# Optimization experiments

Measured on AMD Instinct MI355X. Metric: run time of the kernel, lower is better.

## Reference

```python
import jax, jax.numpy as jnp
import numpy as np

D_MODEL = 1024
D_HEAD = 64

def setup_inputs() -> dict:
    key = jax.random.key(0)
    ks = jax.random.split(key, 7)
    s = 1.0 / np.sqrt(D_MODEL)
    x = jax.random.normal(ks[0], (4, 4096, D_MODEL), dtype=jnp.float32)
    Wq = jax.random.uniform(ks[1], (D_MODEL, D_HEAD), jnp.float32, -s, s)
    bq = jax.random.uniform(ks[2], (D_HEAD,), jnp.float32, -s, s)
    Wk = jax.random.uniform(ks[3], (D_MODEL, D_HEAD), jnp.float32, -s, s)
    bk = jax.random.uniform(ks[4], (D_HEAD,), jnp.float32, -s, s)
    Wv = jax.random.uniform(ks[5], (D_MODEL, D_HEAD), jnp.float32, -s, s)
    bv = jax.random.uniform(ks[6], (D_HEAD,), jnp.float32, -s, s)
    return {"x": x, "Wq": Wq, "bq": bq, "Wk": Wk, "bk": bk, "Wv": Wv, "bv": bv}

def reference(x, Wq, bq, Wk, bk, Wv, bv):
    # x: [b, s, d_model] -> Q,K,V: [b, s, d_head]
    Q = jnp.einsum('bsd,dh->bsh', x, Wq) + bq
    K = jnp.einsum('bsd,dh->bsh', x, Wk) + bk
    V = jnp.einsum('bsd,dh->bsh', x, Wv) + bv
    scale = 1.0 / jnp.sqrt(jnp.asarray(D_HEAD, x.dtype))
    scores = jnp.einsum('bqh,bkh->bqk', Q, K) * scale  # [b, s, s]
    attn = jax.nn.softmax(scores, axis=-1)
    return jnp.einsum('bqk,bkh->bqh', attn, V)  # [b, s, d_head]
```

## Files before the change

### kernel.cpp

```cpp
#include <hip/hip_runtime.h>

typedef __bf16 bf16x8 __attribute__((ext_vector_type(8)));
typedef __bf16 bf16x4 __attribute__((ext_vector_type(4)));
typedef float f32x4 __attribute__((ext_vector_type(4)));
typedef unsigned short u16x8 __attribute__((ext_vector_type(8)));

union FragU { u16x8 u; bf16x8 b; };
union PackU { bf16x4 v; unsigned long long q; };

__device__ __forceinline__ unsigned short bfbits(float f) {
  __bf16 h = (__bf16)f;
  union { __bf16 h; unsigned short s; } cv; cv.h = h;
  return cv.s;
}

#define MFMA16(a, b, c) __builtin_amdgcn_mfma_f32_16x16x32_bf16((a), (b), (c), 0, 0, 0)

#define QSCALE 0.18033688011112042f

__global__ __launch_bounds__(256) void wt_kernel(
    const float* __restrict__ Wq, const float* __restrict__ Wk, const float* __restrict__ Wv,
    unsigned short* __restrict__ WF)
{
  const int m = blockIdx.x >> 5;
  const int c = blockIdx.x & 31;
  const float* W = (m == 0) ? Wq : ((m == 1) ? Wk : Wv);
  const int t = threadIdx.x >> 6;
  const int lane = threadIdx.x & 63;
  const int l15 = lane & 15;
  const int g = lane >> 4;
  unsigned short* dst = WF + ((((size_t)m * 32 + c) * 4 + t) * 64 + lane) * 8;
#pragma unroll
  for (int e = 0; e < 8; ++e)
    dst[e] = bfbits(W[(size_t)(32 * c + 8 * g + e) * 64 + (16 * t + l15)]);
}

__global__ __launch_bounds__(256, 1) void proj_kernel(
    const float* __restrict__ x, const unsigned short* __restrict__ WF,
    const float* __restrict__ bq, const float* __restrict__ bk, const float* __restrict__ bv,
    unsigned short* __restrict__ Qb, unsigned short* __restrict__ KF,
    unsigned short* __restrict__ VF)
{
  __shared__ __align__(16) unsigned short ldsW[4][6144];
  const int tid = threadIdx.x;
  const int lane = tid & 63;
  const int wid = tid >> 6;
  const int l15 = lane & 15;
  const int g = lane >> 4;
  const int row0 = blockIdx.x * 64 + wid * 16;

  f32x4 accQ[4], accK[4], accV[4];
  const f32x4 zero = {0.f, 0.f, 0.f, 0.f};
#pragma unroll
  for (int i = 0; i < 4; ++i) { accQ[i] = zero; accK[i] = zero; accV[i] = zero; }

  const float* xrow = x + (size_t)(row0 + l15) * 1024;
  f32x4 xx0[4], xx1[4];

#define WDMA(CC) { const int sl_ = (CC) & 3; \
    _Pragma("unroll") for (int m_ = 0; m_ < 3; ++m_) { \
      const unsigned short* gs_ = WF + ((((size_t)m_ * 32 + (CC)) * 4 + wid) * 64 + lane) * 8; \
      __builtin_amdgcn_global_load_lds( \
          (const __attribute__((address_space(1))) void*)gs_, \
          (__attribute__((address_space(3))) void*)&ldsW[sl_][(m_ * 4 + wid) * 512], \
          16, 0, 0); } }

#define PLDX(XB, C) { xx0[XB] = *(const f32x4*)(xrow + 32 * (C) + 8 * g); \
                      xx1[XB] = *(const f32x4*)(xrow + 32 * (C) + 8 * g + 4); }

#define SUBIT(CC, KK, WIMM, DOW, DOX) { \
    asm volatile("s_waitcnt vmcnt(" #WIMM ")" ::: "memory"); \
    __builtin_amdgcn_s_barrier(); \
    __builtin_amdgcn_sched_barrier(0); \
    if (DOW) WDMA((CC) + 3); \
    FragU xf; \
    _Pragma("unroll") for (int i_ = 0; i_ < 4; ++i_) { \
      xf.b[i_] = (__bf16)xx0[KK][i_]; xf.b[4 + i_] = (__bf16)xx1[KK][i_]; } \
    if (DOX) PLDX(KK, (CC) + 4); \
    { const int rs_ = (CC) & 3; \
      _Pragma("unroll") for (int t = 0; t < 4; ++t) { \
        const bf16x8 wq_ = *(const bf16x8*)&ldsW[rs_][(0 * 4 + t) * 512 + lane * 8]; \
        const bf16x8 wk_ = *(const bf16x8*)&ldsW[rs_][(1 * 4 + t) * 512 + lane * 8]; \
        const bf16x8 wv_ = *(const bf16x8*)&ldsW[rs_][(2 * 4 + t) * 512 + lane * 8]; \
        accQ[t] = MFMA16(xf.b, wq_, accQ[t]); \
        accK[t] = MFMA16(xf.b, wk_, accK[t]); \
        accV[t] = MFMA16(wv_, xf.b, accV[t]); } } }

  WDMA(0)
  __builtin_amdgcn_sched_barrier(0);
  WDMA(1) WDMA(2)
  PLDX(0, 0) PLDX(1, 1) PLDX(2, 2) PLDX(3, 3)

#pragma unroll 1
  for (int cb = 0; cb < 28; cb += 4) {
    SUBIT(cb + 0, 0, 10, 1, 1)
    SUBIT(cb + 1, 1, 10, 1, 1)
    SUBIT(cb + 2, 2, 10, 1, 1)
    SUBIT(cb + 3, 3, 10, 1, 1)
  }
  SUBIT(28, 0, 10, 1, 0)
  SUBIT(29, 1, 8, 0, 0)
  SUBIT(30, 2, 3, 0, 0)
  SUBIT(31, 3, 0, 0, 0)

  const int b = blockIdx.x >> 6;
  const int kt = blockIdx.x & 63;
  const int q0 = row0 & 4095;
  unsigned short* Qbase = Qb + (size_t)b * 4096 * 64;
#pragma unroll
  for (int t = 0; t < 4; ++t) {
    const int hh = 16 * t + l15;
    const float bqv = bq[hh];
#pragma unroll
    for (int r = 0; r < 4; ++r)
      Qbase[(size_t)(q0 + 4 * g + r) * 64 + hh] = bfbits((accQ[t][r] + bqv) * QSCALE);
  }
  unsigned short* KFb = KF + ((size_t)b * 64 + kt) * 4096;
  unsigned short* VFb = VF + ((size_t)b * 64 + kt) * 4096;
#pragma unroll
  for (int t = 0; t < 4; ++t) {
    const int hh = 16 * t + l15;
    const float bkv = bk[hh];
#pragma unroll
    for (int r = 0; r < 4; ++r) {
      KFb[(size_t)((wid * 2 + (t >> 1)) * 64 + (t & 1) * 32 + (l15 >> 3) * 16 + 4 * g + r) * 8 +
          (l15 & 7)] = bfbits(accK[t][r] + bkv);
      const int hv = 16 * t + 4 * g + r;
      VFb[(size_t)((t * 2 + (wid >> 1)) * 64 + (wid & 1) * 32 + (l15 >> 3) * 16 + 4 * g + r) * 8 +
          (l15 & 7)] = bfbits(accV[t][r] + bv[hv]);
    }
  }
}

__global__ __launch_bounds__(512, 2) void flash_kernel(
    const unsigned short* __restrict__ Qb, const unsigned short* __restrict__ KF,
    const unsigned short* __restrict__ VF, float* __restrict__ out)
{
  __shared__ __align__(16) unsigned char lds[36864];
  const int tid = threadIdx.x;
  const int lane = tid & 63;
  const int w = tid >> 6;
  const int qg = w >> 2;
  const int ks = w & 3;
  const int l15 = lane & 15;
  const int g = lane >> 4;
  const int bid = blockIdx.x;
  const int xcd = bid & 7;
  const int b = xcd >> 1;
  const int qt = (bid >> 3) * 2 + (xcd & 1);
  const int q0 = qt * 64 + qg * 32;

  const unsigned short* Qp = Qb + (size_t)b * 4096 * 64;
  const unsigned short* KFb = KF + (size_t)b * 262144;
  const unsigned short* VFb = VF + (size_t)b * 262144;

  const bf16x8 qfA0 = *(const bf16x8*)(Qp + (size_t)(q0 + l15) * 64 + 8 * g);
  const bf16x8 qfA1 = *(const bf16x8*)(Qp + (size_t)(q0 + l15) * 64 + 32 + 8 * g);
  const bf16x8 qfB0 = *(const bf16x8*)(Qp + (size_t)(q0 + 16 + l15) * 64 + 8 * g);
  const bf16x8 qfB1 = *(const bf16x8*)(Qp + (size_t)(q0 + 16 + l15) * 64 + 32 + 8 * g);

  f32x4 O_A[4], O_B[4];
  const f32x4 zero = {0.f, 0.f, 0.f, 0.f};
#pragma unroll
  for (int i = 0; i < 4; ++i) { O_A[i] = zero; O_B[i] = zero; }
  float mA = -INFINITY, lA = 0.f, mB = -INFINITY, lB = 0.f;
  unsigned short* PwA = (unsigned short*)lds + (w * 2 + 0) * 1152;
  unsigned short* PwB = (unsigned short*)lds + (w * 2 + 1) * 1152;

#define SM_HALF(S, mvar, lvar, OA, PW) { \
  float mt = fmaxf(fmaxf(S[0][0], S[0][1]), fmaxf(S[0][2], S[0][3])); \
  _Pragma("unroll") for (int t = 1; t < 4; ++t) \
    _Pragma("unroll") for (int r = 0; r < 4; ++r) mt = fmaxf(mt, S[t][r]); \
  mt = fmaxf(mt, __shfl_xor(mt, 16)); \
  mt = fmaxf(mt, __shfl_xor(mt, 32)); \
  if (!__all(mt <= mvar + 8.0f)) { \
    const float mnew = fmaxf(mvar, mt); \
    const float alpha = __builtin_amdgcn_exp2f(mvar - mnew); \
    mvar = mnew; lvar *= alpha; \
    _Pragma("unroll") for (int r = 0; r < 4; ++r) { \
      const float ar = __shfl(alpha, 4 * g + r); \
      OA[0][r] *= ar; OA[1][r] *= ar; OA[2][r] *= ar; OA[3][r] *= ar; } \
  } \
  float ps = 0.f; \
  _Pragma("unroll") for (int t = 0; t < 4; ++t) { \
    const float p0 = __builtin_amdgcn_exp2f(S[t][0] - mvar); \
    const float p1 = __builtin_amdgcn_exp2f(S[t][1] - mvar); \
    const float p2 = __builtin_amdgcn_exp2f(S[t][2] - mvar); \
    const float p3 = __builtin_amdgcn_exp2f(S[t][3] - mvar); \
    ps += (p0 + p1) + (p2 + p3); \
    PackU pk_; pk_.v[0] = (__bf16)p0; pk_.v[1] = (__bf16)p1; \
    pk_.v[2] = (__bf16)p2; pk_.v[3] = (__bf16)p3; \
    *(unsigned long long*)((PW) + l15 * 72 + 16 * t + 4 * g) = pk_.q; } \
  ps += __shfl_xor(ps, 16); \
  ps += __shfl_xor(ps, 32); \
  lvar += ps; }

#define FBODY(KT, KFC, KFN, DOLD) { \
    const unsigned short* Vt_ = VFb + (KT) * 4096; \
    bf16x8 vf[8]; \
    _Pragma("unroll") for (int j = 0; j < 8; ++j) \
      vf[j] = *(const bf16x8*)(Vt_ + (j * 64 + lane) * 8); \
    if (DOLD) { \
      const unsigned short* Ktn_ = KFb + ((KT) + 4) * 4096; \
      _Pragma("unroll") for (int j = 0; j < 8; ++j) \
        KFN[j] = *(const bf16x8*)(Ktn_ + (j * 64 + lane) * 8); \
    } \
    f32x4 S_A[4], S_B[4]; \
    _Pragma("unroll") for (int t = 0; t < 4; ++t) { \
      S_A[t] = zero; \
      S_A[t] = MFMA16(KFC[2 * t], qfA0, S_A[t]); \
      S_A[t] = MFMA16(KFC[2 * t + 1], qfA1, S_A[t]); \
      S_B[t] = zero; \
      S_B[t] = MFMA16(KFC[2 * t], qfB0, S_B[t]); \
      S_B[t] = MFMA16(KFC[2 * t + 1], qfB1, S_B[t]); \
    } \
    SM_HALF(S_A, mA, lA, O_A, PwA) \
    SM_HALF(S_B, mB, lB, O_B, PwB) \
    _Pragma("unroll") for (int s = 0; s < 2; ++s) { \
      const bf16x8 paA = *(const bf16x8*)(PwA + l15 * 72 + 32 * s + 8 * g); \
      const bf16x8 paB = *(const bf16x8*)(PwB + l15 * 72 + 32 * s + 8 * g); \
      _Pragma("unroll") for (int nt = 0; nt < 4; ++nt) { \
        O_A[nt] = MFMA16(paA, vf[2 * nt + s], O_A[nt]); \
        O_B[nt] = MFMA16(paB, vf[2 * nt + s], O_B[nt]); \
      } } }

  bf16x8 kfA[8], kfB[8];
  {
    const unsigned short* Kt0 = KFb + ks * 4096;
#pragma unroll
    for (int j = 0; j < 8; ++j) kfA[j] = *(const bf16x8*)(Kt0 + (j * 64 + lane) * 8);
  }
#pragma unroll 1
  for (int kt = ks; kt < 64; kt += 8) {
    FBODY(kt, kfA, kfB, 1)
    FBODY(kt + 4, kfB, kfA, (kt + 8 < 64))
  }

  float* O_l = (float*)lds;
  float* mlp = (float*)(lds + 34816);
  const int q = tid >> 4;
  const int h0 = (tid & 15) * 4;
  const int qh = q >> 4, qr = q & 15;

#pragma unroll 1
  for (int pass = 0; pass < 2; ++pass) {
    __syncthreads();
    if (qg == pass) {
#pragma unroll
      for (int nt = 0; nt < 4; ++nt)
#pragma unroll
        for (int r = 0; r < 4; ++r) {
          O_l[((ks * 2 + 0) * 16 + 4 * g + r) * 68 + 16 * nt + l15] = O_A[nt][r];
          O_l[((ks * 2 + 1) * 16 + 4 * g + r) * 68 + 16 * nt + l15] = O_B[nt][r];
        }
      if (g == 0) {
        mlp[((ks * 2 + 0) * 16 + l15) * 2] = mA; mlp[((ks * 2 + 0) * 16 + l15) * 2 + 1] = lA;
        mlp[((ks * 2 + 1) * 16 + l15) * 2] = mB; mlp[((ks * 2 + 1) * 16 + l15) * 2 + 1] = lB;
      }
    }
    __syncthreads();
    float M = -INFINITY;
#pragma unroll
    for (int s = 0; s < 4; ++s) M = fmaxf(M, mlp[((s * 2 + qh) * 16 + qr) * 2]);
    float L = 0.f;
    f32x4 a0 = zero;
#pragma unroll
    for (int s = 0; s < 4; ++s) {
      const int rowi = (s * 2 + qh) * 16 + qr;
      const float wgt = __builtin_amdgcn_exp2f(mlp[rowi * 2] - M);
      L += wgt * mlp[rowi * 2 + 1];
      const f32x4 o0 = *(const f32x4*)&O_l[rowi * 68 + h0];
#pragma unroll
      for (int i = 0; i < 4; ++i) a0[i] += wgt * o0[i];
    }
    const float inv = 1.0f / L;
    float* ob = out + ((size_t)b * 4096 + qt * 64 + pass * 32 + q) * 64 + h0;
    f32x4 r0 = {a0[0] * inv, a0[1] * inv, a0[2] * inv, a0[3] * inv};
    *(f32x4*)ob = r0;
  }
}

extern "C" void kernel_launch(void* const* d_in, const int* in_sizes, int n_in,
                              void* d_out, int out_size, void* d_ws, size_t ws_size,
                              hipStream_t stream) {
  const float* x  = (const float*)d_in[0];
  const float* Wq = (const float*)d_in[1];
  const float* bq = (const float*)d_in[2];
  const float* Wk = (const float*)d_in[3];
  const float* bk = (const float*)d_in[4];
  const float* Wv = (const float*)d_in[5];
  const float* bv = (const float*)d_in[6];

  char* ws = (char*)d_ws;
  unsigned short* WF = (unsigned short*)ws;
  unsigned short* Qb = (unsigned short*)(ws + (512u << 10));
  unsigned short* KF = (unsigned short*)(ws + (512u << 10) + (2u << 20));
  unsigned short* VF = (unsigned short*)(ws + (512u << 10) + (4u << 20));
  float* out = (float*)d_out;

  hipLaunchKernelGGL(wt_kernel,    dim3(96),  dim3(256), 0, stream, Wq, Wk, Wv, WF);
  hipLaunchKernelGGL(proj_kernel,  dim3(256), dim3(256), 0, stream, x, WF, bq, bk, bv, Qb, KF, VF);
  hipLaunchKernelGGL(flash_kernel, dim3(256), dim3(512), 0, stream, Qb, KF, VF, out);
}
```

Measured before the change: 55.34 us.

## Give each wave private triple-buffered weight LDS copies to drop block barriers

Each wave now DMA-loads all twelve weight fragments for a chunk into its own LDS region, triple-buffered, instead of the four waves sharing one cooperatively loaded copy. This removes the per-chunk s_barrier, so waves synchronise only on their own vmcnt. In exchange each wave issues four times as many global-to-LDS loads, LDS use triples, and prefetch depth drops from three chunks ahead to two. The loop is also fully unrolled.

```diff
diff --git a/kernel.cpp b/kernel.cpp
--- a/kernel.cpp
+++ b/kernel.cpp
@@ -41,7 +41,7 @@
     unsigned short* __restrict__ Qb, unsigned short* __restrict__ KF,
     unsigned short* __restrict__ VF)
 {
-  __shared__ __align__(16) unsigned short ldsW[4][6144];
+  __shared__ __align__(16) unsigned short ldsW[4][3][6144];
   const int tid = threadIdx.x;
   const int lane = tid & 63;
   const int wid = tid >> 6;
@@ -57,51 +57,50 @@
   const float* xrow = x + (size_t)(row0 + l15) * 1024;
   f32x4 xx0[4], xx1[4];
 
-#define WDMA(CC) { const int sl_ = (CC) & 3; \
-    _Pragma("unroll") for (int m_ = 0; m_ < 3; ++m_) { \
-      const unsigned short* gs_ = WF + ((((size_t)m_ * 32 + (CC)) * 4 + wid) * 64 + lane) * 8; \
+#define WDMA(CC) { \
+    _Pragma("unroll") for (int f_ = 0; f_ < 12; ++f_) { \
+      const int m_ = f_ >> 2, t_ = f_ & 3; \
+      const unsigned short* gs_ = WF + ((((size_t)m_ * 32 + (CC)) * 4 + t_) * 64 + lane) * 8; \
       __builtin_amdgcn_global_load_lds( \
           (const __attribute__((address_space(1))) void*)gs_, \
-          (__attribute__((address_space(3))) void*)&ldsW[sl_][(m_ * 4 + wid) * 512], \
+          (__attribute__((address_space(3))) void*)&ldsW[wid][(CC) % 3][f_ * 512], \
           16, 0, 0); } }
 
 #define PLDX(XB, C) { xx0[XB] = *(const f32x4*)(xrow + 32 * (C) + 8 * g); \
                       xx1[XB] = *(const f32x4*)(xrow + 32 * (C) + 8 * g + 4); }
 
-#define SUBIT(CC, KK, WIMM, DOW, DOX) { \
+#define SUBIT(CC, WIMM, DOW, DOX) { \
     asm volatile("s_waitcnt vmcnt(" #WIMM ")" ::: "memory"); \
-    __builtin_amdgcn_s_barrier(); \
     __builtin_amdgcn_sched_barrier(0); \
-    if (DOW) WDMA((CC) + 3); \
+    if (DOW) WDMA((CC) + 2); \
     FragU xf; \
     _Pragma("unroll") for (int i_ = 0; i_ < 4; ++i_) { \
-      xf.b[i_] = (__bf16)xx0[KK][i_]; xf.b[4 + i_] = (__bf16)xx1[KK][i_]; } \
-    if (DOX) PLDX(KK, (CC) + 4); \
-    { const int rs_ = (CC) & 3; \
-      _Pragma("unroll") for (int t = 0; t < 4; ++t) { \
-        const bf16x8 wq_ = *(const bf16x8*)&ldsW[rs_][(0 * 4 + t) * 512 + lane * 8]; \
-        const bf16x8 wk_ = *(const bf16x8*)&ldsW[rs_][(1 * 4 + t) * 512 + lane * 8]; \
-        const bf16x8 wv_ = *(const bf16x8*)&ldsW[rs_][(2 * 4 + t) * 512 + lane * 8]; \
+      xf.b[i_] = (__bf16)xx0[(CC) & 3][i_]; xf.b[4 + i_] = (__bf16)xx1[(CC) & 3][i_]; } \
+    if (DOX) PLDX((CC) & 3, (CC) + 4); \
+    { _Pragma("unroll") for (int t = 0; t < 4; ++t) { \
+        const bf16x8 wq_ = *(const bf16x8*)&ldsW[wid][(CC) % 3][(0 * 4 + t) * 512 + lane * 8]; \
+        const bf16x8 wk_ = *(const bf16x8*)&ldsW[wid][(CC) % 3][(1 * 4 + t) * 512 + lane * 8]; \
+        const bf16x8 wv_ = *(const bf16x8*)&ldsW[wid][(CC) % 3][(2 * 4 + t) * 512 + lane * 8]; \
         accQ[t] = MFMA16(xf.b, wq_, accQ[t]); \
         accK[t] = MFMA16(xf.b, wk_, accK[t]); \
         accV[t] = MFMA16(wv_, xf.b, accV[t]); } } }
 
+#define SUB3(C0) SUBIT(C0, 14, 1, 1) SUBIT(C0 + 1, 14, 1, 1) SUBIT(C0 + 2, 14, 1, 1)
+
+  PLDX(0, 0) PLDX(1, 1) PLDX(2, 2) PLDX(3, 3)
   WDMA(0)
   __builtin_amdgcn_sched_barrier(0);
-  WDMA(1) WDMA(2)
-  PLDX(0, 0) PLDX(1, 1) PLDX(2, 2) PLDX(3, 3)
-
-#pragma unroll 1
-  for (int cb = 0; cb < 28; cb += 4) {
-    SUBIT(cb + 0, 0, 10, 1, 1)
-    SUBIT(cb + 1, 1, 10, 1, 1)
-    SUBIT(cb + 2, 2, 10, 1, 1)
-    SUBIT(cb + 3, 3, 10, 1, 1)
-  }
-  SUBIT(28, 0, 10, 1, 0)
-  SUBIT(29, 1, 8, 0, 0)
-  SUBIT(30, 2, 3, 0, 0)
-  SUBIT(31, 3, 0, 0, 0)
+  WDMA(1)
+
+  SUBIT(0, 10, 1, 1)
+  SUBIT(1, 12, 1, 1)
+  SUBIT(2, 14, 1, 1)
+  SUB3(3) SUB3(6) SUB3(9) SUB3(12) SUB3(15) SUB3(18) SUB3(21) SUB3(24)
+  SUBIT(27, 14, 1, 1)
+  SUBIT(28, 14, 1, 0)
+  SUBIT(29, 12, 1, 0)
+  SUBIT(30, 10, 0, 0)
+  SUBIT(31, 0, 0, 0)
 
   const int b = blockIdx.x >> 6;
   const int kt = blockIdx.x & 63;
```

Measured after the change: 61.65 us. 11.4% more time.
